# Optimization experiments

Hardware: AMD Instinct MI355X
Metric: run time of the kernel (lower is better)

Reference implementation:

```python
import jax, jax.numpy as jnp
import numpy as np

N_NODES = 100000
N_EDGES = 1600000
HIDDEN = 128
OUT_DIM = 1
N_GRAPHS = 2048
VOCAB = 28  # atom types, Embedding(28, hidden_dim)


def setup_inputs() -> dict:
    key = jax.random.key(0)
    ks = jax.random.split(key, 14)
    s = 1.0 / np.sqrt(HIDDEN)
    inp = {
        "x_idx": jax.random.randint(ks[0], (N_NODES,), 0, VOCAB, dtype=jnp.int32),
        "edge_src": jax.random.randint(ks[1], (N_EDGES,), 0, N_NODES, dtype=jnp.int32),
        "edge_dst": jax.random.randint(ks[2], (N_EDGES,), 0, N_NODES, dtype=jnp.int32),
        "batch": jnp.sort(jax.random.randint(ks[3], (N_NODES,), 0, N_GRAPHS, dtype=jnp.int32)),
        # parameters
        "embed": jax.random.normal(ks[4], (VOCAB, HIDDEN), dtype=jnp.float32) * 0.02,
        "eps0": jnp.zeros((1,), dtype=jnp.float32),
        "w1_0": jax.random.normal(ks[5], (HIDDEN, HIDDEN), dtype=jnp.float32) * s,
        "b1_0": jnp.zeros((HIDDEN,), dtype=jnp.float32),
        "w2_0": jax.random.normal(ks[6], (HIDDEN, HIDDEN), dtype=jnp.float32) * s,
        "b2_0": jnp.zeros((HIDDEN,), dtype=jnp.float32),
        "eps1": jnp.zeros((1,), dtype=jnp.float32),
        "w1_1": jax.random.normal(ks[7], (HIDDEN, HIDDEN), dtype=jnp.float32) * s,
        "b1_1": jnp.zeros((HIDDEN,), dtype=jnp.float32),
        "w2_1": jax.random.normal(ks[8], (HIDDEN, OUT_DIM), dtype=jnp.float32) * s,
        "b2_1": jnp.zeros((OUT_DIM,), dtype=jnp.float32),
    }
    return inp


def _gin_layer(x, edge_src, edge_dst, eps, w1, b1, w2, b2):
    # A @ x via edge-list SpMM: out[dst] += x[src]  (same math as to_dense().matmul(x))
    agg = jax.ops.segment_sum(x[edge_src], edge_dst, num_segments=N_NODES)
    h = agg + (1.0 + eps) * x  # [N, in_feats]; eps broadcasts (shape [1])
    h = h @ w1 + b1            # linear1 (no nonlinearity between, as in source)
    return h @ w2 + b2         # linear2


def reference(x_idx, edge_src, edge_dst, batch, embed,
              eps0, w1_0, b1_0, w2_0, b2_0,
              eps1, w1_1, b1_1, w2_1, b2_1):
    x = embed[x_idx]  # [N, HIDDEN] — Embedding lookup (.squeeze(1) trivial here)
    x = jax.nn.relu(_gin_layer(x, edge_src, edge_dst, eps0, w1_0, b1_0, w2_0, b2_0))
    x = _gin_layer(x, edge_src, edge_dst, eps1, w1_1, b1_1, w2_1, b2_1)  # [N, 1]
    y_hat = jax.ops.segment_sum(x.squeeze(-1), batch, num_segments=N_GRAPHS)  # [G]
    return (y_hat, x)
```

## Files before the change

### kernel.cpp

```cpp
#include <hip/hip_runtime.h>

#define N_NODES  100000
#define N_EDGES  1600000
#define HIDDEN   128
#define N_GRAPHS 2048
#define VOCAB    28
#define NB       392
#define CAP      5000
#define NBIN     512
#define EPB      3125
#define EPT      7
#define CSTR     29

__global__ __launch_bounds__(256) void k_init(float* __restrict__ out,
                                              int* __restrict__ gcursor) {
    int i = blockIdx.x * 256 + threadIdx.x;
    if (i < N_GRAPHS) out[i] = 0.0f;
    else if (i < N_GRAPHS + NB) gcursor[i - N_GRAPHS] = 0;
}

__global__ __launch_bounds__(512) void k_binprep(const int* __restrict__ esrc,
                                                 const int* __restrict__ edst,
                                                 const int* __restrict__ x_idx,
                                                 unsigned* __restrict__ binned,
                                                 int* __restrict__ gcursor,
                                                 const float* __restrict__ embed,
                                                 const float* __restrict__ w1_0,
                                                 const float* __restrict__ w2_0,
                                                 const float* __restrict__ b1_0,
                                                 const float* __restrict__ b2_0,
                                                 const float* __restrict__ w1_1,
                                                 const float* __restrict__ b1_1,
                                                 const float* __restrict__ w2_1,
                                                 const float* __restrict__ b2_1,
                                                 float* __restrict__ T,
                                                 float* __restrict__ bc0,
                                                 float* __restrict__ wc1,
                                                 float* __restrict__ bc1) {
    const int tid = threadIdx.x;
    const int bid = blockIdx.x;

    if (bid >= NBIN) {
        if (bid < NBIN + 7) {
            int g = (bid - NBIN) * 512 + tid;
            int i = g >> 7, j = g & 127;
            float s = 0.f;
#pragma unroll 8
            for (int k = 0; k < HIDDEN; ++k)
                s += embed[i * HIDDEN + k] * w1_0[k * HIDDEN + j];
            T[g] = s;
        } else {
            if (tid < 128) {
                float s = 0.f;
#pragma unroll 8
                for (int k = 0; k < HIDDEN; ++k)
                    s += b1_0[k] * w2_0[k * HIDDEN + tid];
                bc0[tid] = s + b2_0[tid];
                if (tid == 0) {
                    float q = 0.f;
                    for (int k = 0; k < HIDDEN; ++k) q += b1_1[k] * w2_1[k];
                    bc1[0] = q + b2_1[0];
                }
            } else if (tid < 256) {
                int i = tid - 128;
                float s = 0.f;
#pragma unroll 8
                for (int k = 0; k < HIDDEN; ++k)
                    s += w1_1[i * HIDDEN + k] * w2_1[k];
                wc1[i] = s;
            }
        }
        return;
    }

    __shared__ int hist[512];
    __shared__ int scanbuf[512];
    __shared__ int lbase[512];
    __shared__ int lcur[512];
    __shared__ int gbase[512];
    __shared__ unsigned stage[EPB];
    __shared__ int tgt[EPB];

    hist[tid] = 0;
    lcur[tid] = 0;
    __syncthreads();

    unsigned mypk[EPT];
    short    myb[EPT];
#pragma unroll
    for (int i = 0; i < EPT; ++i) {
        int idx = i * 512 + tid;
        myb[i] = -1;
        if (idx < EPB) {
            int e   = bid * EPB + idx;
            int dst = edst[e];
            int src = esrc[e];
            int b   = dst >> 8;
            int dl  = dst & 255;
            int vix = x_idx[src];
            mypk[i] = ((unsigned)dl << 22) | ((unsigned)vix << 17) | (unsigned)src;
            myb[i]  = (short)b;
            atomicAdd(&hist[b], 1);
        }
    }
    __syncthreads();

    int v = hist[tid];
    scanbuf[tid] = v;
    __syncthreads();
    for (int off = 1; off < 512; off <<= 1) {
        int x = (tid >= off) ? scanbuf[tid - off] : 0;
        __syncthreads();
        scanbuf[tid] += x;
        __syncthreads();
    }
    lbase[tid] = scanbuf[tid] - v;
    if (tid < NB) gbase[tid] = (v > 0) ? atomicAdd(&gcursor[tid], v) : 0;
    __syncthreads();

#pragma unroll
    for (int i = 0; i < EPT; ++i) {
        if (myb[i] >= 0) {
            int b   = myb[i];
            int pos = lbase[b] + atomicAdd(&lcur[b], 1);
            stage[pos] = mypk[i];
            tgt[pos]   = (b << 12) | (pos - lbase[b]);
        }
    }
    __syncthreads();

    for (int i = tid; i < EPB; i += 512) {
        int u = tgt[i];
        int b = u >> 12, lr = u & 4095;
        binned[b * CAP + gbase[b] + lr] = stage[i];
    }
}

__global__ __launch_bounds__(512) void k_prep2(const float* __restrict__ T,
                                               const float* __restrict__ w2_0,
                                               float* __restrict__ EW) {
    int g = blockIdx.x * 512 + threadIdx.x;
    if (g >= VOCAB * HIDDEN) return;
    int i = g >> 7, j = g & 127;
    float s = 0.f;
#pragma unroll 8
    for (int k = 0; k < HIDDEN; ++k)
        s += T[i * HIDDEN + k] * w2_0[k * HIDDEN + j];
    EW[g] = s;
}

__global__ __launch_bounds__(256) void k_layerC(const unsigned* __restrict__ binned,
                                                const int* __restrict__ gcursor,
                                                const int* __restrict__ x_idx,
                                                const float* __restrict__ EW,
                                                const float* __restrict__ bc0,
                                                const float* __restrict__ wc1,
                                                const float* __restrict__ eps0,
                                                float* __restrict__ d) {
    __shared__ int lcnt[256 * CSTR];

    const int tid = threadIdx.x;
    const int b   = blockIdx.x;

    for (int i = tid; i < 256 * CSTR; i += 256) lcnt[i] = 0;
    __syncthreads();

    const int cnt = gcursor[b];
    const unsigned* bp = binned + (size_t)b * CAP;
    for (int i = tid; i < cnt; i += 256) {
        unsigned pk = bp[i];
        atomicAdd(&lcnt[(pk >> 22) * CSTR + ((pk >> 17) & 31)], 1);
    }
    __syncthreads();

    const int n      = b * 256 + tid;
    const bool valid = (n < N_NODES);
    const int xi     = valid ? x_idx[n] : 0;
    const float s    = 1.0f + eps0[0];

    float cf[VOCAB];
#pragma unroll
    for (int v = 0; v < VOCAB; ++v)
        cf[v] = (float)lcnt[tid * CSTR + v] + ((v == xi) ? s : 0.0f);

    const float4* EW4 = reinterpret_cast<const float4*>(EW);
    const float4* b04 = reinterpret_cast<const float4*>(bc0);
    const float4* w14 = reinterpret_cast<const float4*>(wc1);

    float dacc = 0.f;
#pragma unroll 1
    for (int f4 = 0; f4 < 32; ++f4) {
        float4 a = b04[f4];
#pragma unroll
        for (int v = 0; v < VOCAB; ++v) {
            float4 e = EW4[v * 32 + f4];
            a.x += cf[v] * e.x;
            a.y += cf[v] * e.y;
            a.z += cf[v] * e.z;
            a.w += cf[v] * e.w;
        }
        float4 w = w14[f4];
        dacc += fmaxf(a.x, 0.f) * w.x + fmaxf(a.y, 0.f) * w.y
              + fmaxf(a.z, 0.f) * w.z + fmaxf(a.w, 0.f) * w.w;
    }
    if (valid) d[n] = dacc;
}

__global__ __launch_bounds__(256) void k_B2(const unsigned* __restrict__ binned,
                                            const int* __restrict__ gcursor,
                                            const float* __restrict__ d,
                                            const int* __restrict__ batch,
                                            const float* __restrict__ eps1,
                                            const float* __restrict__ bc1,
                                            float* __restrict__ out) {
    __shared__ float racc[256];
    __shared__ float gacc[N_GRAPHS];

    const int tid = threadIdx.x;
    const int b   = blockIdx.x;
    const int n0  = b * 256;
    if (n0 >= N_NODES) return;
    const int nlast = min(n0 + 255, N_NODES - 1);

    racc[tid] = 0.f;
    const int g0 = batch[n0];
    const int g1 = batch[nlast];
    for (int g = g0 + tid; g <= g1; g += 256) gacc[g] = 0.f;
    __syncthreads();

    const int cnt = gcursor[b];
    const unsigned* bp = binned + (size_t)b * CAP;
    for (int i = tid; i < cnt; i += 256) {
        unsigned pk = bp[i];
        atomicAdd(&racc[pk >> 22], d[pk & 0x1FFFFu]);
    }
    __syncthreads();

    int n = n0 + tid;
    if (n < N_NODES) {
        float r = (1.0f + eps1[0]) * d[n] + racc[tid] + bc1[0];
        out[N_GRAPHS + n] = r;
        atomicAdd(&gacc[batch[n]], r);
    }
    __syncthreads();
    for (int g = g0 + tid; g <= g1; g += 256) {
        float v = gacc[g];
        if (v != 0.f) atomicAdd(&out[g], v);
    }
}

extern "C" void kernel_launch(void* const* d_in, const int* in_sizes, int n_in,
                              void* d_out, int out_size, void* d_ws, size_t ws_size,
                              hipStream_t stream) {
    const int*   x_idx = (const int*)d_in[0];
    const int*   esrc  = (const int*)d_in[1];
    const int*   edst  = (const int*)d_in[2];
    const int*   batch = (const int*)d_in[3];
    const float* embed = (const float*)d_in[4];
    const float* eps0  = (const float*)d_in[5];
    const float* w1_0  = (const float*)d_in[6];
    const float* b1_0  = (const float*)d_in[7];
    const float* w2_0  = (const float*)d_in[8];
    const float* b2_0  = (const float*)d_in[9];
    const float* eps1  = (const float*)d_in[10];
    const float* w1_1  = (const float*)d_in[11];
    const float* b1_1  = (const float*)d_in[12];
    const float* w2_1  = (const float*)d_in[13];
    const float* b2_1  = (const float*)d_in[14];

    float* out = (float*)d_out;

    int*      gcursor = (int*)d_ws;
    unsigned* binned  = (unsigned*)(gcursor + 512);
    float*    d       = (float*)(binned + (size_t)NB * CAP);
    float*    T       = d + 100352;
    float*    bc0     = T + VOCAB * HIDDEN;
    float*    wc1     = bc0 + HIDDEN;
    float*    bc1     = wc1 + HIDDEN;
    float*    EW      = bc1 + 1;

    k_init<<<(N_GRAPHS + NB + 255) / 256, 256, 0, stream>>>(out, gcursor);

    k_binprep<<<NBIN + 8, 512, 0, stream>>>(esrc, edst, x_idx, binned, gcursor,
                                            embed, w1_0, w2_0, b1_0, b2_0,
                                            w1_1, b1_1, w2_1, b2_1,
                                            T, bc0, wc1, bc1);

    k_prep2<<<7, 512, 0, stream>>>(T, w2_0, EW);

    k_layerC<<<NB, 256, 0, stream>>>(binned, gcursor, x_idx, EW, bc0, wc1, eps0, d);

    k_B2<<<NB, 256, 0, stream>>>(binned, gcursor, d, batch, eps1, bc1, out);
}
```

Before: 168.9 us.

## Rebin nodes into 256 blocks of 392 with 1024-thread blocks, drop LDS staging

Changes node partitioning from 392 bins of 256 nodes to 256 bins of 392 nodes, using magic-multiply division, so each bin maps to one block on the 256 CUs. All kernels move to 1024-thread blocks. In binning, the scan plus LDS staging pass is replaced by direct scattered global writes using per-bin atomic cursors, which removes shared-memory work and barriers but loses write coalescing. In layerC only 392 of 1024 threads do the dense per-node compute, so most threads sit idle in that phase.

```diff
diff --git a/kernel.cpp b/kernel.cpp
--- a/kernel.cpp
+++ b/kernel.cpp
@@ -5,12 +5,14 @@
 #define HIDDEN   128
 #define N_GRAPHS 2048
 #define VOCAB    28
-#define NB       392
-#define CAP      5000
+#define NB       256
+#define NPB      392
+#define CAP      7000
 #define NBIN     512
 #define EPB      3125
-#define EPT      7
+#define EPT      4
 #define CSTR     29
+#define MAGIC    2804876602ULL
 
 __global__ __launch_bounds__(256) void k_init(float* __restrict__ out,
                                               int* __restrict__ gcursor) {
@@ -19,36 +21,38 @@
     else if (i < N_GRAPHS + NB) gcursor[i - N_GRAPHS] = 0;
 }
 
-__global__ __launch_bounds__(512) void k_binprep(const int* __restrict__ esrc,
-                                                 const int* __restrict__ edst,
-                                                 const int* __restrict__ x_idx,
-                                                 unsigned* __restrict__ binned,
-                                                 int* __restrict__ gcursor,
-                                                 const float* __restrict__ embed,
-                                                 const float* __restrict__ w1_0,
-                                                 const float* __restrict__ w2_0,
-                                                 const float* __restrict__ b1_0,
-                                                 const float* __restrict__ b2_0,
-                                                 const float* __restrict__ w1_1,
-                                                 const float* __restrict__ b1_1,
-                                                 const float* __restrict__ w2_1,
-                                                 const float* __restrict__ b2_1,
-                                                 float* __restrict__ T,
-                                                 float* __restrict__ bc0,
-                                                 float* __restrict__ wc1,
-                                                 float* __restrict__ bc1) {
+__global__ __launch_bounds__(1024) void k_binprep(const int* __restrict__ esrc,
+                                                  const int* __restrict__ edst,
+                                                  const int* __restrict__ x_idx,
+                                                  unsigned* __restrict__ binned,
+                                                  int* __restrict__ gcursor,
+                                                  const float* __restrict__ embed,
+                                                  const float* __restrict__ w1_0,
+                                                  const float* __restrict__ w2_0,
+                                                  const float* __restrict__ b1_0,
+                                                  const float* __restrict__ b2_0,
+                                                  const float* __restrict__ w1_1,
+                                                  const float* __restrict__ b1_1,
+                                                  const float* __restrict__ w2_1,
+                                                  const float* __restrict__ b2_1,
+                                                  float* __restrict__ T,
+                                                  float* __restrict__ bc0,
+                                                  float* __restrict__ wc1,
+                                                  float* __restrict__ bc1) {
     const int tid = threadIdx.x;
     const int bid = blockIdx.x;
 
     if (bid >= NBIN) {
-        if (bid < NBIN + 7) {
-            int g = (bid - NBIN) * 512 + tid;
-            int i = g >> 7, j = g & 127;
-            float s = 0.f;
-#pragma unroll 8
-            for (int k = 0; k < HIDDEN; ++k)
-                s += embed[i * HIDDEN + k] * w1_0[k * HIDDEN + j];
-            T[g] = s;
+        if (bid < NBIN + 4) {
+            int g = (bid - NBIN) * 1024 + tid;
+            if (g < VOCAB * HIDDEN) {
+                int i = g >> 7, j = g & 127;
+                float s = 0.f;
+#pragma unroll 8
+                for (int k = 0; k < HIDDEN; ++k)
+                    s += embed[i * HIDDEN + k] * w1_0[k * HIDDEN + j];
+                T[g] = s;
+            }
         } else {
             if (tid < 128) {
                 float s = 0.f;
@@ -73,30 +77,25 @@
         return;
     }
 
-    __shared__ int hist[512];
-    __shared__ int scanbuf[512];
-    __shared__ int lbase[512];
-    __shared__ int lcur[512];
-    __shared__ int gbase[512];
-    __shared__ unsigned stage[EPB];
-    __shared__ int tgt[EPB];
-
-    hist[tid] = 0;
-    lcur[tid] = 0;
+    __shared__ int hist[NB];
+    __shared__ int lcur[NB];
+    __shared__ int gbase[NB];
+
+    if (tid < NB) { hist[tid] = 0; lcur[tid] = 0; }
     __syncthreads();
 
     unsigned mypk[EPT];
     short    myb[EPT];
 #pragma unroll
     for (int i = 0; i < EPT; ++i) {
-        int idx = i * 512 + tid;
+        int idx = i * 1024 + tid;
         myb[i] = -1;
         if (idx < EPB) {
             int e   = bid * EPB + idx;
             int dst = edst[e];
             int src = esrc[e];
-            int b   = dst >> 8;
-            int dl  = dst & 255;
+            int b   = (int)(((unsigned long long)dst * MAGIC) >> 40);
+            int dl  = dst - b * NPB;
             int vix = x_idx[src];
             mypk[i] = ((unsigned)dl << 22) | ((unsigned)vix << 17) | (unsigned)src;
             myb[i]  = (short)b;
@@ -105,41 +104,26 @@
     }
     __syncthreads();
 
-    int v = hist[tid];
-    scanbuf[tid] = v;
-    __syncthreads();
-    for (int off = 1; off < 512; off <<= 1) {
-        int x = (tid >= off) ? scanbuf[tid - off] : 0;
-        __syncthreads();
-        scanbuf[tid] += x;
-        __syncthreads();
-    }
-    lbase[tid] = scanbuf[tid] - v;
-    if (tid < NB) gbase[tid] = (v > 0) ? atomicAdd(&gcursor[tid], v) : 0;
+    if (tid < NB) {
+        int v = hist[tid];
+        gbase[tid] = (v > 0) ? atomicAdd(&gcursor[tid], v) : 0;
+    }
     __syncthreads();
 
 #pragma unroll
     for (int i = 0; i < EPT; ++i) {
         if (myb[i] >= 0) {
-            int b   = myb[i];
-            int pos = lbase[b] + atomicAdd(&lcur[b], 1);
-            stage[pos] = mypk[i];
-            tgt[pos]   = (b << 12) | (pos - lbase[b]);
-        }
-    }
-    __syncthreads();
-
-    for (int i = tid; i < EPB; i += 512) {
-        int u = tgt[i];
-        int b = u >> 12, lr = u & 4095;
-        binned[b * CAP + gbase[b] + lr] = stage[i];
-    }
-}
-
-__global__ __launch_bounds__(512) void k_prep2(const float* __restrict__ T,
-                                               const float* __restrict__ w2_0,
-                                               float* __restrict__ EW) {
-    int g = blockIdx.x * 512 + threadIdx.x;
+            int b  = myb[i];
+            int lr = atomicAdd(&lcur[b], 1);
+            binned[(size_t)b * CAP + gbase[b] + lr] = mypk[i];
+        }
+    }
+}
+
+__global__ __launch_bounds__(1024) void k_prep2(const float* __restrict__ T,
+                                                const float* __restrict__ w2_0,
+                                                float* __restrict__ EW) {
+    int g = blockIdx.x * 1024 + threadIdx.x;
     if (g >= VOCAB * HIDDEN) return;
     int i = g >> 7, j = g & 127;
     float s = 0.f;
@@ -149,31 +133,33 @@
     EW[g] = s;
 }
 
-__global__ __launch_bounds__(256) void k_layerC(const unsigned* __restrict__ binned,
-                                                const int* __restrict__ gcursor,
-                                                const int* __restrict__ x_idx,
-                                                const float* __restrict__ EW,
-                                                const float* __restrict__ bc0,
-                                                const float* __restrict__ wc1,
-                                                const float* __restrict__ eps0,
-                                                float* __restrict__ d) {
-    __shared__ int lcnt[256 * CSTR];
+__global__ __launch_bounds__(1024) void k_layerC(const unsigned* __restrict__ binned,
+                                                 const int* __restrict__ gcursor,
+                                                 const int* __restrict__ x_idx,
+                                                 const float* __restrict__ EW,
+                                                 const float* __restrict__ bc0,
+                                                 const float* __restrict__ wc1,
+                                                 const float* __restrict__ eps0,
+                                                 float* __restrict__ d) {
+    __shared__ int lcnt[NPB * CSTR];
 
     const int tid = threadIdx.x;
     const int b   = blockIdx.x;
 
-    for (int i = tid; i < 256 * CSTR; i += 256) lcnt[i] = 0;
+    for (int i = tid; i < NPB * CSTR; i += 1024) lcnt[i] = 0;
     __syncthreads();
 
     const int cnt = gcursor[b];
     const unsigned* bp = binned + (size_t)b * CAP;
-    for (int i = tid; i < cnt; i += 256) {
+    for (int i = tid; i < cnt; i += 1024) {
         unsigned pk = bp[i];
         atomicAdd(&lcnt[(pk >> 22) * CSTR + ((pk >> 17) & 31)], 1);
     }
     __syncthreads();
 
-    const int n      = b * 256 + tid;
+    if (tid >= NPB) return;
+
+    const int n      = b * NPB + tid;
     const bool valid = (n < N_NODES);
     const int xi     = valid ? x_idx[n] : 0;
     const float s    = 1.0f + eps0[0];
@@ -206,44 +192,43 @@
     if (valid) d[n] = dacc;
 }
 
-__global__ __launch_bounds__(256) void k_B2(const unsigned* __restrict__ binned,
-                                            const int* __restrict__ gcursor,
-                                            const float* __restrict__ d,
-                                            const int* __restrict__ batch,
-                                            const float* __restrict__ eps1,
-                                            const float* __restrict__ bc1,
-                                            float* __restrict__ out) {
-    __shared__ float racc[256];
+__global__ __launch_bounds__(1024) void k_B2(const unsigned* __restrict__ binned,
+                                             const int* __restrict__ gcursor,
+                                             const float* __restrict__ d,
+                                             const int* __restrict__ batch,
+                                             const float* __restrict__ eps1,
+                                             const float* __restrict__ bc1,
+                                             float* __restrict__ out) {
+    __shared__ float racc[NPB];
     __shared__ float gacc[N_GRAPHS];
 
     const int tid = threadIdx.x;
     const int b   = blockIdx.x;
-    const int n0  = b * 256;
-    if (n0 >= N_NODES) return;
-    const int nlast = min(n0 + 255, N_NODES - 1);
-
-    racc[tid] = 0.f;
+    const int n0  = b * NPB;
+    const int nlast = min(n0 + NPB - 1, N_NODES - 1);
+
+    if (tid < NPB) racc[tid] = 0.f;
     const int g0 = batch[n0];
     const int g1 = batch[nlast];
-    for (int g = g0 + tid; g <= g1; g += 256) gacc[g] = 0.f;
+    for (int g = g0 + tid; g <= g1; g += 1024) gacc[g] = 0.f;
     __syncthreads();
 
     const int cnt = gcursor[b];
     const unsigned* bp = binned + (size_t)b * CAP;
-    for (int i = tid; i < cnt; i += 256) {
+    for (int i = tid; i < cnt; i += 1024) {
         unsigned pk = bp[i];
         atomicAdd(&racc[pk >> 22], d[pk & 0x1FFFFu]);
     }
     __syncthreads();
 
     int n = n0 + tid;
-    if (n < N_NODES) {
+    if (tid < NPB && n < N_NODES) {
         float r = (1.0f + eps1[0]) * d[n] + racc[tid] + bc1[0];
         out[N_GRAPHS + n] = r;
         atomicAdd(&gacc[batch[n]], r);
     }
     __syncthreads();
-    for (int g = g0 + tid; g <= g1; g += 256) {
+    for (int g = g0 + tid; g <= g1; g += 1024) {
         float v = gacc[g];
         if (v != 0.f) atomicAdd(&out[g], v);
     }
@@ -279,16 +264,16 @@
     float*    bc1     = wc1 + HIDDEN;
     float*    EW      = bc1 + 1;
 
-    k_init<<<(N_GRAPHS + NB + 255) / 256, 256, 0, stream>>>(out, gcursor);
-
-    k_binprep<<<NBIN + 8, 512, 0, stream>>>(esrc, edst, x_idx, binned, gcursor,
-                                            embed, w1_0, w2_0, b1_0, b2_0,
-                                            w1_1, b1_1, w2_1, b2_1,
-                                            T, bc0, wc1, bc1);
-
-    k_prep2<<<7, 512, 0, stream>>>(T, w2_0, EW);
-
-    k_layerC<<<NB, 256, 0, stream>>>(binned, gcursor, x_idx, EW, bc0, wc1, eps0, d);
-
-    k_B2<<<NB, 256, 0, stream>>>(binned, gcursor, d, batch, eps1, bc1, out);
-}
+    k_init<<<9, 256, 0, stream>>>(out, gcursor);
+
+    k_binprep<<<NBIN + 5, 1024, 0, stream>>>(esrc, edst, x_idx, binned, gcursor,
+                                             embed, w1_0, w2_0, b1_0, b2_0,
+                                             w1_1, b1_1, w2_1, b2_1,
+                                             T, bc0, wc1, bc1);
+
+    k_prep2<<<4, 1024, 0, stream>>>(T, w2_0, EW);
+
+    k_layerC<<<NB, 1024, 0, stream>>>(binned, gcursor, x_idx, EW, bc0, wc1, eps0, d);
+
+    k_B2<<<NB, 1024, 0, stream>>>(binned, gcursor, d, batch, eps1, bc1, out);
+}
```

New measurement: 164.8 us. -2.5%, faster.
